# Kernel optimization log

Hardware: AMD Instinct MI355X
Metric: run time of the kernel (lower is better)

## Reference

```python
import jax, jax.numpy as jnp
import numpy as np

B, N = 4, 2048
VD, CD = 256, 64
H = 4
INNER = VD  # inner_ratio = 1
D = INNER // H  # head_dim = 64
EPS = 1e-5
RMS_EPS = 1e-6


def layer_norm(x, g, b):
    m = jnp.mean(x, axis=-1, keepdims=True)
    v = jnp.mean((x - m) ** 2, axis=-1, keepdims=True)
    return (x - m) * jax.lax.rsqrt(v + EPS) * g + b


def rms_norm(x, s):
    ms = jnp.mean(x * x, axis=-1, keepdims=True)
    return x * jax.lax.rsqrt(ms + RMS_EPS) * s


def split_heads(x):  # (b, n, h*d) -> (b, h, n, d)
    b, n, _ = x.shape
    return x.reshape(b, n, H, D).transpose(0, 2, 1, 3)


def setup_inputs() -> dict:
    key = jax.random.key(0)
    ks = jax.random.split(key, 10)
    w = lambda k, shp: jax.random.normal(k, shp, dtype=jnp.float32) * 0.02
    return {
        "V": jax.random.normal(ks[0], (B, N, VD), dtype=jnp.float32),
        "C": jax.random.normal(ks[1], (B, N, CD), dtype=jnp.float32),
        "vn_g": jnp.ones((VD,), jnp.float32), "vn_b": jnp.zeros((VD,), jnp.float32),
        "cn_g": jnp.ones((CD,), jnp.float32), "cn_b": jnp.zeros((CD,), jnp.float32),
        "W_vqk": w(ks[2], (VD, 2 * INNER)), "b_vqk": jnp.zeros((2 * INNER,), jnp.float32),
        "rms_v": jnp.ones((2 * INNER,), jnp.float32),
        "W_cqk": w(ks[3], (CD, 2 * INNER)), "b_cqk": jnp.zeros((2 * INNER,), jnp.float32),
        "rms_c": jnp.ones((2 * INNER,), jnp.float32),
        "W_vv": w(ks[4], (VD, INNER)), "b_vv": jnp.zeros((INNER,), jnp.float32),
        "W_cv": w(ks[5], (CD, INNER)), "b_cv": jnp.zeros((INNER,), jnp.float32),
        "W_ov": w(ks[6], (INNER, VD)), "b_ov": jnp.zeros((VD,), jnp.float32),
        "W_oc": w(ks[7], (INNER, CD)), "b_oc": jnp.zeros((CD,), jnp.float32),
    }


def reference(V, C, vn_g, vn_b, cn_g, cn_b, W_vqk, b_vqk, rms_v, W_cqk, b_cqk, rms_c,
              W_vv, b_vv, W_cv, b_cv, W_ov, b_ov, W_oc, b_oc):
    Vn = layer_norm(V, vn_g, vn_b)
    Cn = layer_norm(C, cn_g, cn_b)
    qkv = rms_norm(Vn @ W_vqk + b_vqk, rms_v)
    qkc = rms_norm(Cn @ W_cqk + b_cqk, rms_c)
    qv, kv = jnp.split(qkv, 2, axis=-1)
    qc, kc = jnp.split(qkc, 2, axis=-1)
    vv = Vn @ W_vv + b_vv
    vc = Cn @ W_cv + b_cv
    qv, kv, vv, qc, kc, vc = map(split_heads, (qv, kv, vv, qc, kc, vc))
    # shared attention map: softmax((QvKv^T + QcKc^T)/sqrt(d))
    scores = (jnp.einsum("bhnd,bhmd->bhnm", qv, kv)
              + jnp.einsum("bhnd,bhmd->bhnm", qc, kc)) / np.sqrt(D).astype(np.float32)
    attn = jax.nn.softmax(scores, axis=-1)
    out_v = jnp.einsum("bhnm,bhmd->bhnd", attn, vv).transpose(0, 2, 1, 3).reshape(B, N, INNER)
    out_c = jnp.einsum("bhnm,bhmd->bhnd", attn, vc).transpose(0, 2, 1, 3).reshape(B, N, INNER)
    return out_v @ W_ov + b_ov, out_c @ W_oc + b_oc
```

## Files before the change

### kernel.cpp

```cpp
#include <hip/hip_runtime.h>

typedef unsigned short u16;
typedef unsigned int   u32;
typedef short s16x8 __attribute__((ext_vector_type(8)));
typedef float f32x4 __attribute__((ext_vector_type(4)));

#define WS_STATSV 0
#define WS_STATSC 65536
#define WS_WT_VQK 131072
#define WS_WT_CQK 393216
#define WS_WT_VV  458752
#define WS_WT_CV  589824
#define WS_WT_OV  622592
#define WS_WT_OC  753664
#define WS_Q      786432
#define WS_K      9175040
#define WS_VT     17563648
#define WS_OV     25952256
#define WS_OC     30146560

__device__ __forceinline__ float bf2f(u16 h){
  union { u32 u; float f; } x; x.u = ((u32)h) << 16; return x.f;
}
__device__ __forceinline__ u16 f2bf(float f){
  union { float f; u32 u; } x; x.f = f;
  u32 u = x.u; u += 0x7fffu + ((u >> 16) & 1u);
  return (u16)(u >> 16);
}
__device__ __forceinline__ f32x4 mfma16(s16x8 a, s16x8 b, f32x4 c){
  return __builtin_amdgcn_mfma_f32_16x16x32_bf16(a, b, c, 0, 0, 0);
}
__device__ __forceinline__ void async16(const u16* g, u16* l){
  __builtin_amdgcn_global_load_lds(
      (const __attribute__((address_space(1))) u32*)(const void*)g,
      (__attribute__((address_space(3))) u32*)(void*)l, 16, 0, 0);
}

__global__ __launch_bounds__(256) void k_prep(const float* V, const float* C,
    const float* Wvqk, const float* Wcqk, const float* Wvv, const float* Wcv,
    const float* Wov, const float* Woc, char* ws){
  int bid = blockIdx.x;
  if (bid < 4096){
    int wid = threadIdx.x >> 6, lane = threadIdx.x & 63;
    float2* sV = (float2*)(ws + WS_STATSV);
    float2* sC = (float2*)(ws + WS_STATSC);
    float s = 0.f, s2 = 0.f; int row; float2* dst; float invn;
    if (bid < 2048){
      row = bid*4 + wid;
      const float4* p = (const float4*)(V + row*256);
      float4 v = p[lane];
      s = v.x+v.y+v.z+v.w; s2 = v.x*v.x+v.y*v.y+v.z*v.z+v.w*v.w;
      dst = sV; invn = 1.0f/256.0f;
    } else {
      row = (bid-2048)*4 + wid;
      float x = C[row*64 + lane];
      s = x; s2 = x*x;
      dst = sC; invn = 1.0f/64.0f;
    }
    for (int d=1; d<64; d<<=1){ s += __shfl_xor(s,d); s2 += __shfl_xor(s2,d); }
    if (lane == 0){
      float m = s*invn; float var = s2*invn - m*m; if (var < 0.f) var = 0.f;
      float rstd = rsqrtf(var + 1e-5f);
      float2 o; o.x = rstd; o.y = -m*rstd;
      dst[row] = o;
    }
  } else {
    int tb = bid - 4096;
    const float* src; u16* dst; int K, N, rel;
    if      (tb <  64){ src=Wvqk; dst=(u16*)(ws+WS_WT_VQK); K=256; N=512; rel=tb;     }
    else if (tb <  80){ src=Wcqk; dst=(u16*)(ws+WS_WT_CQK); K=64;  N=512; rel=tb-64;  }
    else if (tb < 112){ src=Wvv;  dst=(u16*)(ws+WS_WT_VV);  K=256; N=256; rel=tb-80;  }
    else if (tb < 120){ src=Wcv;  dst=(u16*)(ws+WS_WT_CV);  K=64;  N=256; rel=tb-112; }
    else if (tb < 152){ src=Wov;  dst=(u16*)(ws+WS_WT_OV);  K=256; N=256; rel=tb-120; }
    else              { src=Woc;  dst=(u16*)(ws+WS_WT_OC);  K=256; N=64;  rel=tb-152; }
    int e = rel*2048 + threadIdx.x*8;
    int k = e / N, n0 = e % N;
    float4 t0 = *(const float4*)(src + e);
    float4 t1 = *(const float4*)(src + e + 4);
    dst[(n0+0)*K + k] = f2bf(t0.x);
    dst[(n0+1)*K + k] = f2bf(t0.y);
    dst[(n0+2)*K + k] = f2bf(t0.z);
    dst[(n0+3)*K + k] = f2bf(t0.w);
    dst[(n0+4)*K + k] = f2bf(t1.x);
    dst[(n0+5)*K + k] = f2bf(t1.y);
    dst[(n0+6)*K + k] = f2bf(t1.z);
    dst[(n0+7)*K + k] = f2bf(t1.w);
  }
}

__device__ __forceinline__ s16x8 ln_frag(const float* A, const float* g, const float* bb,
                                         int base, int k0, float2 stt){
  float4 x0 = *(const float4*)(A + base + k0);
  float4 x1 = *(const float4*)(A + base + k0 + 4);
  float4 g0 = *(const float4*)(g + k0);
  float4 g1 = *(const float4*)(g + k0 + 4);
  float4 b0 = *(const float4*)(bb + k0);
  float4 b1 = *(const float4*)(bb + k0 + 4);
  s16x8 af;
  af[0] = (short)f2bf(fmaf(fmaf(x0.x, stt.x, stt.y), g0.x, b0.x));
  af[1] = (short)f2bf(fmaf(fmaf(x0.y, stt.x, stt.y), g0.y, b0.y));
  af[2] = (short)f2bf(fmaf(fmaf(x0.z, stt.x, stt.y), g0.z, b0.z));
  af[3] = (short)f2bf(fmaf(fmaf(x0.w, stt.x, stt.y), g0.w, b0.w));
  af[4] = (short)f2bf(fmaf(fmaf(x1.x, stt.x, stt.y), g1.x, b1.x));
  af[5] = (short)f2bf(fmaf(fmaf(x1.y, stt.x, stt.y), g1.y, b1.y));
  af[6] = (short)f2bf(fmaf(fmaf(x1.z, stt.x, stt.y), g1.z, b1.z));
  af[7] = (short)f2bf(fmaf(fmaf(x1.w, stt.x, stt.y), g1.w, b1.w));
  return af;
}

__global__ __launch_bounds__(256) void k_proj(const float* V, const float* C,
    const float* vg, const float* vb, const float* cgam, const float* cbet,
    const float* bvqk, const float* bcqk, const float* rmsv, const float* rmsc,
    const float* bvv, const float* bcv, char* ws){
  __shared__ float ssl[4][16];
  int bid = blockIdx.x;
  int tid = threadIdx.x, lane = tid & 63, w = tid >> 6;
  int c = lane & 15, q = lane >> 4;

  if (bid < 1024){
    bool csd = bid >= 512;
    int rb = (bid & 511) * 16;
    const float* A   = csd ? C : V;
    int K            = csd ? 64 : 256;
    const float2* st = (const float2*)(ws + (csd ? WS_STATSC : WS_STATSV));
    const float* g   = csd ? cgam : vg;
    const float* bb  = csd ? cbet : vb;
    const u16* Wt    = (const u16*)(ws + (csd ? WS_WT_CQK : WS_WT_VQK));
    const float* bias= csd ? bcqk : bvqk;
    const float* rms = csd ? rmsc : rmsv;
    int dOff         = csd ? 64 : 0;

    int row = rb + c;
    float2 stt = st[row];
    int j0 = w * 128;

    f32x4 acc[8];
    #pragma unroll
    for (int f=0; f<8; f++){ f32x4 z = {0.f,0.f,0.f,0.f}; acc[f] = z; }

    int nkc = K >> 5;
    for (int kc=0; kc<nkc; kc++){
      int k0 = kc*32 + q*8;
      s16x8 af = ln_frag(A, g, bb, row*K, k0, stt);
      #pragma unroll
      for (int f=0; f<8; f++){
        s16x8 bfr = *(const s16x8*)(Wt + (j0 + f*16 + c)*K + k0);
        acc[f] = mfma16(af, bfr, acc[f]);
      }
    }

    float ss[4] = {0.f,0.f,0.f,0.f};
    float rsv[8];
    #pragma unroll
    for (int f=0; f<8; f++){
      int j = j0 + f*16 + c;
      float bsv = bias[j]; rsv[f] = rms[j];
      #pragma unroll
      for (int i=0;i<4;i++){ acc[f][i] += bsv; ss[i] += acc[f][i]*acc[f][i]; }
    }
    #pragma unroll
    for (int d=1; d<16; d<<=1){
      #pragma unroll
      for (int i=0;i<4;i++) ss[i] += __shfl_xor(ss[i], d);
    }
    if (c == 0){
      #pragma unroll
      for (int i=0;i<4;i++) ssl[w][q*4 + i] = ss[i];
    }
    __syncthreads();
    float rmsr[4];
    #pragma unroll
    for (int i=0;i<4;i++){
      int rl = q*4 + i;
      float tot = ssl[0][rl] + ssl[1][rl] + ssl[2][rl] + ssl[3][rl];
      rmsr[i] = rsqrtf(tot * (1.0f/512.0f) + 1e-6f);
    }
    u16* dstb = (u16*)(ws + (w < 2 ? WS_Q : WS_K));
    float qs = (w < 2) ? 0.125f*1.44269504f : 1.0f;
    #pragma unroll
    for (int f=0; f<8; f++){
      int jj = (j0 + f*16 + c) & 255;
      int head = jj >> 6, dd = (jj & 63) + dOff;
      #pragma unroll
      for (int i=0;i<4;i++){
        int r = rb + q*4 + i;
        int b_ = r >> 11, n = r & 2047;
        dstb[((b_*4 + head)*2048 + n)*128 + dd] = f2bf(acc[f][i]*rmsr[i]*rsv[f]*qs);
      }
    }
  } else {
    int vb2 = bid - 1024;
    bool csd = vb2 >= 256;
    int rb = (vb2 & 255) * 32;
    const float* A   = csd ? C : V;
    int K            = csd ? 64 : 256;
    const float2* st = (const float2*)(ws + (csd ? WS_STATSC : WS_STATSV));
    const float* g   = csd ? cgam : vg;
    const float* bb  = csd ? cbet : vb;
    const u16* Wt    = (const u16*)(ws + (csd ? WS_WT_CV : WS_WT_VV));
    const float* bias= csd ? bcv : bvv;
    int dOff         = csd ? 64 : 0;

    int s = w & 1, cgp = w >> 1;
    int r0 = rb + s*16, row = r0 + c;
    float2 stt = st[row];
    int j0 = cgp * 128;

    f32x4 acc[8];
    #pragma unroll
    for (int f=0; f<8; f++){ f32x4 z = {0.f,0.f,0.f,0.f}; acc[f] = z; }

    int nkc = K >> 5;
    for (int kc=0; kc<nkc; kc++){
      int k0 = kc*32 + q*8;
      s16x8 af = ln_frag(A, g, bb, row*K, k0, stt);
      #pragma unroll
      for (int f=0; f<8; f++){
        s16x8 bfr = *(const s16x8*)(Wt + (j0 + f*16 + c)*K + k0);
        acc[f] = mfma16(af, bfr, acc[f]);
      }
    }
    u16* vt = (u16*)(ws + WS_VT);
    int r = r0 + q*4;
    int b_ = r >> 11, n = r & 2047;
    int m = n & 31;
    int nper = (n & ~31) | (((m & 15) >> 2)*8 + (m >> 4)*4);
    #pragma unroll
    for (int f=0; f<8; f++){
      int j = j0 + f*16 + c;
      float bv_ = bias[j];
      int head = j >> 6, dd = (j & 63) + dOff;
      ushort4 pk;
      pk.x = f2bf(acc[f][0] + bv_); pk.y = f2bf(acc[f][1] + bv_);
      pk.z = f2bf(acc[f][2] + bv_); pk.w = f2bf(acc[f][3] + bv_);
      *(ushort4*)(vt + ((b_*4 + head)*128 + dd)*2048 + nper) = pk;
    }
  }
}

__global__ __launch_bounds__(256, 2) void k_attn(char* ws){
  const u16* Qw = (const u16*)(ws + WS_Q);
  const u16* Kw = (const u16*)(ws + WS_K);
  const u16* Vt = (const u16*)(ws + WS_VT);
  u16* Ov = (u16*)(ws + WS_OV);
  u16* Oc = (u16*)(ws + WS_OC);
  __shared__ char smem[65536];
  u16* sm16 = (u16*)smem;

  int bh = blockIdx.x & 15, qb = blockIdx.x >> 4;
  int tid = threadIdx.x, lane = tid & 63, w = tid >> 6;
  int c = lane & 15, q = lane >> 4;
  int g = w & 1, h = w >> 1, ht = tid & 127;
  int qr0 = qb*64 + g*32;

  s16x8 qf[2][4];
  #pragma unroll
  for (int s=0;s<2;s++)
    #pragma unroll
    for (int kc=0;kc<4;kc++)
      qf[s][kc] = *(const s16x8*)(Qw + (bh*2048 + qr0 + s*16 + c)*128 + kc*32 + q*8);

  const u16* ksrc[4]; const u16* vsrc[4];
  #pragma unroll
  for (int i=0;i<4;i++){
    int sc = i*128 + ht;
    { int r = sc >> 4, j = (sc & 15) ^ (r & 15);
      ksrc[i] = Kw + (bh*2048 + r)*128 + j*8; }
    { int r = sc >> 2, j = (sc & 3) ^ ((r >> 1) & 3);
      vsrc[i] = Vt + (bh*128 + r)*2048 + j*8; }
  }

  f32x4 o[2][8];
  float lsum[2] = {0.f, 0.f};
  #pragma unroll
  for (int s=0;s<2;s++)
    #pragma unroll
    for (int f8=0;f8<8;f8++){ f32x4 z = {0.f,0.f,0.f,0.f}; o[s][f8] = z; }

  auto stage = [&](int buf, int t){
    u16* kd = sm16 + (h*2+buf)*4096;
    u16* vd = sm16 + 16384 + (h*2+buf)*4096;
    #pragma unroll
    for (int i=0;i<4;i++){
      async16(ksrc[i] + t*4096, kd + (i*128+ht)*8);
      async16(vsrc[i] + t*32,   vd + (i*128+ht)*8);
    }
  };

  auto step = [&](int bi, int tt){
    int t = h*32 + tt;
    __syncthreads();
    if (tt < 31) stage(bi^1, t+1);

    const u16* kb = sm16 + (h*2+bi)*4096;
    const u16* vb = sm16 + 16384 + (h*2+bi)*4096;
    s16x8 kf[2][4];
    #pragma unroll
    for (int f=0;f<2;f++)
      #pragma unroll
      for (int kc=0;kc<4;kc++)
        kf[f][kc] = *(const s16x8*)(kb + ((f*16+c)*16 + (((kc*4+q) ^ c) & 15))*8);
    s16x8 vf[8];
    #pragma unroll
    for (int f8=0;f8<8;f8++)
      vf[f8] = *(const s16x8*)(vb + ((f8*16+c)*4 + ((q ^ ((c>>1)&3)) & 3))*8);

    f32x4 sfr[2][2];
    #pragma unroll
    for (int s=0;s<2;s++)
      #pragma unroll
      for (int f=0;f<2;f++){ f32x4 z = {0.f,0.f,0.f,0.f}; sfr[s][f] = z; }
    #pragma unroll
    for (int s=0;s<2;s++)
      #pragma unroll
      for (int f=0;f<2;f++)
        #pragma unroll
        for (int kc=0;kc<4;kc++)
          sfr[s][f] = mfma16(kf[f][kc], qf[s][kc], sfr[s][f]);

    #pragma unroll
    for (int s=0;s<2;s++){
      float p0 = exp2f(sfr[s][0][0]), p1 = exp2f(sfr[s][0][1]);
      float p2 = exp2f(sfr[s][0][2]), p3 = exp2f(sfr[s][0][3]);
      float p4 = exp2f(sfr[s][1][0]), p5 = exp2f(sfr[s][1][1]);
      float p6 = exp2f(sfr[s][1][2]), p7 = exp2f(sfr[s][1][3]);
      lsum[s] += ((p0+p1)+(p2+p3)) + ((p4+p5)+(p6+p7));
      union { u32 u[4]; s16x8 v; } pa;
      pa.u[0] = (u32)f2bf(p0) | ((u32)f2bf(p1) << 16);
      pa.u[1] = (u32)f2bf(p2) | ((u32)f2bf(p3) << 16);
      pa.u[2] = (u32)f2bf(p4) | ((u32)f2bf(p5) << 16);
      pa.u[3] = (u32)f2bf(p6) | ((u32)f2bf(p7) << 16);
      #pragma unroll
      for (int f8=0;f8<8;f8++)
        o[s][f8] = mfma16(pa.v, vf[f8], o[s][f8]);
    }
  };

  stage(0, h*32);
  for (int tt=0; tt<32; tt+=2){
    step(0, tt);
    step(1, tt+1);
  }

  __syncthreads();
  float* mg = (float*)smem;
  if (h == 1){
    float* d = mg + (g*64 + lane)*67;
    #pragma unroll
    for (int s=0;s<2;s++)
      #pragma unroll
      for (int f8=0;f8<8;f8++)
        #pragma unroll
        for (int i=0;i<4;i++) d[(s*8+f8)*4 + i] = o[s][f8][i];
    d[64] = lsum[0]; d[65] = lsum[1];
  }
  __syncthreads();
  if (h == 0){
    float* d = mg + (g*64 + lane)*67;
    #pragma unroll
    for (int s=0;s<2;s++)
      #pragma unroll
      for (int f8=0;f8<8;f8++)
        #pragma unroll
        for (int i=0;i<4;i++) o[s][f8][i] += d[(s*8+f8)*4 + i];
    lsum[0] += d[64]; lsum[1] += d[65];

    #pragma unroll
    for (int s=0;s<2;s++){
      lsum[s] += __shfl_xor(lsum[s], 16);
      lsum[s] += __shfl_xor(lsum[s], 32);
    }

    int b_ = bh >> 2, hh = bh & 3;
    #pragma unroll
    for (int s=0;s<2;s++){
      float inv[4];
      #pragma unroll
      for (int i=0;i<4;i++) inv[i] = 1.0f/__shfl(lsum[s], q*4 + i);
      #pragma unroll
      for (int f8=0;f8<8;f8++){
        int col = f8*16 + c;
        u16* dst = (col < 64) ? Ov : Oc;
        int ddim = col & 63;
        #pragma unroll
        for (int i=0;i<4;i++){
          int n = qr0 + s*16 + q*4 + i;
          dst[(b_*2048 + n)*256 + hh*64 + ddim] = f2bf(o[s][f8][i]*inv[i]);
        }
      }
    }
  }
}

__global__ __launch_bounds__(256) void k_out(const u16* Av, const u16* Wtv, const float* bv,
                                             const u16* Ac, const u16* Wtc, const float* bc,
                                             float* out){
  int bid = blockIdx.x;
  int tid = threadIdx.x, lane = tid & 63, w = tid >> 6;
  int c = lane & 15, q = lane >> 4;
  if (bid < 512){
    int rb = bid * 16;
    int row = rb + c;
    int j0 = w * 64;
    f32x4 acc[4];
    #pragma unroll
    for (int f=0; f<4; f++){ f32x4 z = {0.f,0.f,0.f,0.f}; acc[f] = z; }
    for (int kc=0; kc<8; kc++){
      int k0 = kc*32 + q*8;
      s16x8 af = *(const s16x8*)(Av + row*256 + k0);
      #pragma unroll
      for (int f=0; f<4; f++){
        s16x8 bfr = *(const s16x8*)(Wtv + (j0 + f*16 + c)*256 + k0);
        acc[f] = mfma16(af, bfr, acc[f]);
      }
    }
    #pragma unroll
    for (int f=0; f<4; f++){
      int j = j0 + f*16 + c;
      float bb = bv[j];
      #pragma unroll
      for (int i=0;i<4;i++)
        out[(rb + q*4 + i)*256 + j] = acc[f][i] + bb;
    }
  } else {
    int rb = (bid - 512) * 64;
    int r0 = rb + w*16, row = r0 + c;
    f32x4 acc[4];
    #pragma unroll
    for (int f=0; f<4; f++){ f32x4 z = {0.f,0.f,0.f,0.f}; acc[f] = z; }
    for (int kc=0; kc<8; kc++){
      int k0 = kc*32 + q*8;
      s16x8 af = *(const s16x8*)(Ac + row*256 + k0);
      #pragma unroll
      for (int f=0; f<4; f++){
        s16x8 bfr = *(const s16x8*)(Wtc + (f*16 + c)*256 + k0);
        acc[f] = mfma16(af, bfr, acc[f]);
      }
    }
    float* oc = out + 2097152;
    #pragma unroll
    for (int f=0; f<4; f++){
      int j = f*16 + c;
      float bb = bc[j];
      #pragma unroll
      for (int i=0;i<4;i++)
        oc[(r0 + q*4 + i)*64 + j] = acc[f][i] + bb;
    }
  }
}

extern "C" void kernel_launch(void* const* d_in, const int* in_sizes, int n_in,
                              void* d_out, int out_size, void* d_ws, size_t ws_size,
                              hipStream_t stream){
  (void)in_sizes; (void)n_in; (void)out_size; (void)ws_size;
  const float* V    = (const float*)d_in[0];
  const float* C    = (const float*)d_in[1];
  const float* vng  = (const float*)d_in[2];
  const float* vnb  = (const float*)d_in[3];
  const float* cng  = (const float*)d_in[4];
  const float* cnb  = (const float*)d_in[5];
  const float* Wvqk = (const float*)d_in[6];
  const float* bvqk = (const float*)d_in[7];
  const float* rmsv = (const float*)d_in[8];
  const float* Wcqk = (const float*)d_in[9];
  const float* bcqk = (const float*)d_in[10];
  const float* rmsc = (const float*)d_in[11];
  const float* Wvv  = (const float*)d_in[12];
  const float* bvv  = (const float*)d_in[13];
  const float* Wcv  = (const float*)d_in[14];
  const float* bcv  = (const float*)d_in[15];
  const float* Wov  = (const float*)d_in[16];
  const float* bov  = (const float*)d_in[17];
  const float* Woc  = (const float*)d_in[18];
  const float* boc  = (const float*)d_in[19];
  char* ws = (char*)d_ws;
  float* out = (float*)d_out;

  k_prep<<<4256, 256, 0, stream>>>(V, C, Wvqk, Wcqk, Wvv, Wcv, Wov, Woc, ws);
  k_proj<<<1536, 256, 0, stream>>>(V, C, vng, vnb, cng, cnb,
                                   bvqk, bcqk, rmsv, rmsc, bvv, bcv, ws);
  k_attn<<<512, 256, 0, stream>>>(ws);
  k_out<<<640, 256, 0, stream>>>((const u16*)(ws + WS_OV), (const u16*)(ws + WS_WT_OV), bov,
                                 (const u16*)(ws + WS_OC), (const u16*)(ws + WS_WT_OC), boc,
                                 out);
}
```

Before: 215.1 us.

## Pre-pack K/V in MFMA fragment order and load directly from global

The layer norm is now applied once in the prep kernel, which writes normalized bf16 V and C rows into the workspace; the projection kernel reads these instead of recomputing the norm for every column block. The projection kernel now stores K and V directly in the per-lane MFMA fragment order that attention consumes. The attention kernel then drops its LDS staging and barriers and double-buffers tiles in registers with coalesced 16-byte global loads. The trade is higher register pressure in attention and the loss of LDS sharing between waves, so each wave fetches its own K/V tiles from L2. The normalized activations reuse the WS_OV/WS_OC buffers, which attention later overwrites.

```diff
diff --git a/kernel.cpp b/kernel.cpp
--- a/kernel.cpp
+++ b/kernel.cpp
@@ -30,39 +30,39 @@
 __device__ __forceinline__ f32x4 mfma16(s16x8 a, s16x8 b, f32x4 c){
   return __builtin_amdgcn_mfma_f32_16x16x32_bf16(a, b, c, 0, 0, 0);
 }
-__device__ __forceinline__ void async16(const u16* g, u16* l){
-  __builtin_amdgcn_global_load_lds(
-      (const __attribute__((address_space(1))) u32*)(const void*)g,
-      (__attribute__((address_space(3))) u32*)(void*)l, 16, 0, 0);
-}
 
 __global__ __launch_bounds__(256) void k_prep(const float* V, const float* C,
+    const float* vng, const float* vnb, const float* cng, const float* cnb,
     const float* Wvqk, const float* Wcqk, const float* Wvv, const float* Wcv,
     const float* Wov, const float* Woc, char* ws){
   int bid = blockIdx.x;
   if (bid < 4096){
     int wid = threadIdx.x >> 6, lane = threadIdx.x & 63;
-    float2* sV = (float2*)(ws + WS_STATSV);
-    float2* sC = (float2*)(ws + WS_STATSC);
-    float s = 0.f, s2 = 0.f; int row; float2* dst; float invn;
     if (bid < 2048){
-      row = bid*4 + wid;
+      int row = bid*4 + wid;
       const float4* p = (const float4*)(V + row*256);
       float4 v = p[lane];
-      s = v.x+v.y+v.z+v.w; s2 = v.x*v.x+v.y*v.y+v.z*v.z+v.w*v.w;
-      dst = sV; invn = 1.0f/256.0f;
+      float s = v.x+v.y+v.z+v.w, s2 = v.x*v.x+v.y*v.y+v.z*v.z+v.w*v.w;
+      for (int d=1; d<64; d<<=1){ s += __shfl_xor(s,d); s2 += __shfl_xor(s2,d); }
+      float m = s*(1.0f/256.0f); float var = s2*(1.0f/256.0f) - m*m; if (var < 0.f) var = 0.f;
+      float rstd = rsqrtf(var + 1e-5f), nb = -m*rstd;
+      float4 gg = ((const float4*)vng)[lane];
+      float4 bb = ((const float4*)vnb)[lane];
+      ushort4 pk;
+      pk.x = f2bf(fmaf(fmaf(v.x, rstd, nb), gg.x, bb.x));
+      pk.y = f2bf(fmaf(fmaf(v.y, rstd, nb), gg.y, bb.y));
+      pk.z = f2bf(fmaf(fmaf(v.z, rstd, nb), gg.z, bb.z));
+      pk.w = f2bf(fmaf(fmaf(v.w, rstd, nb), gg.w, bb.w));
+      *(ushort4*)((u16*)(ws + WS_OV) + row*256 + lane*4) = pk;
     } else {
-      row = (bid-2048)*4 + wid;
+      int row = (bid-2048)*4 + wid;
       float x = C[row*64 + lane];
-      s = x; s2 = x*x;
-      dst = sC; invn = 1.0f/64.0f;
-    }
-    for (int d=1; d<64; d<<=1){ s += __shfl_xor(s,d); s2 += __shfl_xor(s2,d); }
-    if (lane == 0){
-      float m = s*invn; float var = s2*invn - m*m; if (var < 0.f) var = 0.f;
+      float s = x, s2 = x*x;
+      for (int d=1; d<64; d<<=1){ s += __shfl_xor(s,d); s2 += __shfl_xor(s2,d); }
+      float m = s*(1.0f/64.0f); float var = s2*(1.0f/64.0f) - m*m; if (var < 0.f) var = 0.f;
       float rstd = rsqrtf(var + 1e-5f);
-      float2 o; o.x = rstd; o.y = -m*rstd;
-      dst[row] = o;
+      float xn = fmaf(fmaf(x, rstd, -m*rstd), cng[lane], cnb[lane]);
+      ((u16*)(ws + WS_OC))[row*64 + lane] = f2bf(xn);
     }
   } else {
     int tb = bid - 4096;
@@ -88,30 +88,8 @@
   }
 }
 
-__device__ __forceinline__ s16x8 ln_frag(const float* A, const float* g, const float* bb,
-                                         int base, int k0, float2 stt){
-  float4 x0 = *(const float4*)(A + base + k0);
-  float4 x1 = *(const float4*)(A + base + k0 + 4);
-  float4 g0 = *(const float4*)(g + k0);
-  float4 g1 = *(const float4*)(g + k0 + 4);
-  float4 b0 = *(const float4*)(bb + k0);
-  float4 b1 = *(const float4*)(bb + k0 + 4);
-  s16x8 af;
-  af[0] = (short)f2bf(fmaf(fmaf(x0.x, stt.x, stt.y), g0.x, b0.x));
-  af[1] = (short)f2bf(fmaf(fmaf(x0.y, stt.x, stt.y), g0.y, b0.y));
-  af[2] = (short)f2bf(fmaf(fmaf(x0.z, stt.x, stt.y), g0.z, b0.z));
-  af[3] = (short)f2bf(fmaf(fmaf(x0.w, stt.x, stt.y), g0.w, b0.w));
-  af[4] = (short)f2bf(fmaf(fmaf(x1.x, stt.x, stt.y), g1.x, b1.x));
-  af[5] = (short)f2bf(fmaf(fmaf(x1.y, stt.x, stt.y), g1.y, b1.y));
-  af[6] = (short)f2bf(fmaf(fmaf(x1.z, stt.x, stt.y), g1.z, b1.z));
-  af[7] = (short)f2bf(fmaf(fmaf(x1.w, stt.x, stt.y), g1.w, b1.w));
-  return af;
-}
-
-__global__ __launch_bounds__(256) void k_proj(const float* V, const float* C,
-    const float* vg, const float* vb, const float* cgam, const float* cbet,
-    const float* bvqk, const float* bcqk, const float* rmsv, const float* rmsc,
-    const float* bvv, const float* bcv, char* ws){
+__global__ __launch_bounds__(256) void k_proj(const float* bvqk, const float* bcqk,
+    const float* rmsv, const float* rmsc, const float* bvv, const float* bcv, char* ws){
   __shared__ float ssl[4][16];
   int bid = blockIdx.x;
   int tid = threadIdx.x, lane = tid & 63, w = tid >> 6;
@@ -120,18 +98,14 @@
   if (bid < 1024){
     bool csd = bid >= 512;
     int rb = (bid & 511) * 16;
-    const float* A   = csd ? C : V;
+    const u16* An    = (const u16*)(ws + (csd ? WS_OC : WS_OV));
     int K            = csd ? 64 : 256;
-    const float2* st = (const float2*)(ws + (csd ? WS_STATSC : WS_STATSV));
-    const float* g   = csd ? cgam : vg;
-    const float* bb  = csd ? cbet : vb;
     const u16* Wt    = (const u16*)(ws + (csd ? WS_WT_CQK : WS_WT_VQK));
     const float* bias= csd ? bcqk : bvqk;
     const float* rms = csd ? rmsc : rmsv;
     int dOff         = csd ? 64 : 0;
 
     int row = rb + c;
-    float2 stt = st[row];
     int j0 = w * 128;
 
     f32x4 acc[8];
@@ -141,7 +115,7 @@
     int nkc = K >> 5;
     for (int kc=0; kc<nkc; kc++){
       int k0 = kc*32 + q*8;
-      s16x8 af = ln_frag(A, g, bb, row*K, k0, stt);
+      s16x8 af = *(const s16x8*)(An + row*K + k0);
       #pragma unroll
       for (int f=0; f<8; f++){
         s16x8 bfr = *(const s16x8*)(Wt + (j0 + f*16 + c)*K + k0);
@@ -175,35 +149,49 @@
       float tot = ssl[0][rl] + ssl[1][rl] + ssl[2][rl] + ssl[3][rl];
       rmsr[i] = rsqrtf(tot * (1.0f/512.0f) + 1e-6f);
     }
-    u16* dstb = (u16*)(ws + (w < 2 ? WS_Q : WS_K));
-    float qs = (w < 2) ? 0.125f*1.44269504f : 1.0f;
-    #pragma unroll
-    for (int f=0; f<8; f++){
-      int jj = (j0 + f*16 + c) & 255;
-      int head = jj >> 6, dd = (jj & 63) + dOff;
-      #pragma unroll
-      for (int i=0;i<4;i++){
-        int r = rb + q*4 + i;
-        int b_ = r >> 11, n = r & 2047;
-        dstb[((b_*4 + head)*2048 + n)*128 + dd] = f2bf(acc[f][i]*rmsr[i]*rsv[f]*qs);
+    if (w < 2){
+      u16* dstb = (u16*)(ws + WS_Q);
+      const float qs = 0.125f*1.44269504f;
+      #pragma unroll
+      for (int f=0; f<8; f++){
+        int jj = (j0 + f*16 + c) & 255;
+        int head = jj >> 6, dd = (jj & 63) + dOff;
+        #pragma unroll
+        for (int i=0;i<4;i++){
+          int r = rb + q*4 + i;
+          int b_ = r >> 11, n = r & 2047;
+          dstb[((b_*4 + head)*2048 + n)*128 + dd] = f2bf(acc[f][i]*rmsr[i]*rsv[f]*qs);
+        }
+      }
+    } else {
+      u16* kfb = (u16*)(ws + WS_K);
+      #pragma unroll
+      for (int f=0; f<8; f++){
+        int jj = (j0 + f*16 + c) & 255;
+        int head = jj >> 6, dd = (jj & 63) + dOff;
+        int kcK = dd >> 5, qK = (dd >> 3) & 3, eK = dd & 7;
+        #pragma unroll
+        for (int i=0;i<4;i++){
+          int r = rb + q*4 + i;
+          int b_ = r >> 11, n = r & 2047;
+          int t = n >> 5, fK = (n >> 4) & 1, cK = n & 15;
+          kfb[(b_*4 + head)*262144 + t*4096 + (fK*4 + kcK)*512 + (qK*16 + cK)*8 + eK]
+            = f2bf(acc[f][i]*rmsr[i]*rsv[f]);
+        }
       }
     }
   } else {
     int vb2 = bid - 1024;
     bool csd = vb2 >= 256;
     int rb = (vb2 & 255) * 32;
-    const float* A   = csd ? C : V;
+    const u16* An    = (const u16*)(ws + (csd ? WS_OC : WS_OV));
     int K            = csd ? 64 : 256;
-    const float2* st = (const float2*)(ws + (csd ? WS_STATSC : WS_STATSV));
-    const float* g   = csd ? cgam : vg;
-    const float* bb  = csd ? cbet : vb;
     const u16* Wt    = (const u16*)(ws + (csd ? WS_WT_CV : WS_WT_VV));
     const float* bias= csd ? bcv : bvv;
     int dOff         = csd ? 64 : 0;
 
     int s = w & 1, cgp = w >> 1;
     int r0 = rb + s*16, row = r0 + c;
-    float2 stt = st[row];
     int j0 = cgp * 128;
 
     f32x4 acc[8];
@@ -213,44 +201,45 @@
     int nkc = K >> 5;
     for (int kc=0; kc<nkc; kc++){
       int k0 = kc*32 + q*8;
-      s16x8 af = ln_frag(A, g, bb, row*K, k0, stt);
+      s16x8 af = *(const s16x8*)(An + row*K + k0);
       #pragma unroll
       for (int f=0; f<8; f++){
         s16x8 bfr = *(const s16x8*)(Wt + (j0 + f*16 + c)*K + k0);
         acc[f] = mfma16(af, bfr, acc[f]);
       }
     }
-    u16* vt = (u16*)(ws + WS_VT);
+    u16* vfb = (u16*)(ws + WS_VT);
     int r = r0 + q*4;
     int b_ = r >> 11, n = r & 2047;
-    int m = n & 31;
-    int nper = (n & ~31) | (((m & 15) >> 2)*8 + (m >> 4)*4);
+    int t = n >> 5, m = n & 31;
+    int qV = (m < 16) ? (m >> 2) : ((m >> 2) - 4);
+    int e0 = (m < 16) ? 0 : 4;
     #pragma unroll
     for (int f=0; f<8; f++){
       int j = j0 + f*16 + c;
       float bv_ = bias[j];
       int head = j >> 6, dd = (j & 63) + dOff;
+      int f8 = dd >> 4, cV = dd & 15;
       ushort4 pk;
       pk.x = f2bf(acc[f][0] + bv_); pk.y = f2bf(acc[f][1] + bv_);
       pk.z = f2bf(acc[f][2] + bv_); pk.w = f2bf(acc[f][3] + bv_);
-      *(ushort4*)(vt + ((b_*4 + head)*128 + dd)*2048 + nper) = pk;
+      *(ushort4*)(vfb + (b_*4 + head)*262144 + t*4096 + f8*512 + (qV*16 + cV)*8 + e0) = pk;
     }
   }
 }
 
 __global__ __launch_bounds__(256, 2) void k_attn(char* ws){
   const u16* Qw = (const u16*)(ws + WS_Q);
-  const u16* Kw = (const u16*)(ws + WS_K);
-  const u16* Vt = (const u16*)(ws + WS_VT);
+  const u16* KF = (const u16*)(ws + WS_K);
+  const u16* VF = (const u16*)(ws + WS_VT);
   u16* Ov = (u16*)(ws + WS_OV);
   u16* Oc = (u16*)(ws + WS_OC);
-  __shared__ char smem[65536];
-  u16* sm16 = (u16*)smem;
+  __shared__ float mg[2][64][67];
 
   int bh = blockIdx.x & 15, qb = blockIdx.x >> 4;
   int tid = threadIdx.x, lane = tid & 63, w = tid >> 6;
   int c = lane & 15, q = lane >> 4;
-  int g = w & 1, h = w >> 1, ht = tid & 127;
+  int g = w & 1, h = w >> 1;
   int qr0 = qb*64 + g*32;
 
   s16x8 qf[2][4];
@@ -260,15 +249,8 @@
     for (int kc=0;kc<4;kc++)
       qf[s][kc] = *(const s16x8*)(Qw + (bh*2048 + qr0 + s*16 + c)*128 + kc*32 + q*8);
 
-  const u16* ksrc[4]; const u16* vsrc[4];
-  #pragma unroll
-  for (int i=0;i<4;i++){
-    int sc = i*128 + ht;
-    { int r = sc >> 4, j = (sc & 15) ^ (r & 15);
-      ksrc[i] = Kw + (bh*2048 + r)*128 + j*8; }
-    { int r = sc >> 2, j = (sc & 3) ^ ((r >> 1) & 3);
-      vsrc[i] = Vt + (bh*128 + r)*2048 + j*8; }
-  }
+  const u16* kb = KF + bh*262144 + h*131072 + lane*8;
+  const u16* vb = VF + bh*262144 + h*131072 + lane*8;
 
   f32x4 o[2][8];
   float lsum[2] = {0.f, 0.f};
@@ -277,34 +259,22 @@
     #pragma unroll
     for (int f8=0;f8<8;f8++){ f32x4 z = {0.f,0.f,0.f,0.f}; o[s][f8] = z; }
 
-  auto stage = [&](int buf, int t){
-    u16* kd = sm16 + (h*2+buf)*4096;
-    u16* vd = sm16 + 16384 + (h*2+buf)*4096;
-    #pragma unroll
-    for (int i=0;i<4;i++){
-      async16(ksrc[i] + t*4096, kd + (i*128+ht)*8);
-      async16(vsrc[i] + t*32,   vd + (i*128+ht)*8);
-    }
+  s16x8 kA[2][4], vA[8], kB[2][4], vB[8];
+
+  auto loadT = [&](s16x8 (&kf)[2][4], s16x8 (&vf)[8], int tt){
+    const u16* kt = kb + tt*4096;
+    const u16* vt = vb + tt*4096;
+    #pragma unroll
+    for (int f=0;f<2;f++)
+      #pragma unroll
+      for (int kc=0;kc<4;kc++)
+        kf[f][kc] = *(const s16x8*)(kt + (f*4+kc)*512);
+    #pragma unroll
+    for (int f8=0;f8<8;f8++)
+      vf[f8] = *(const s16x8*)(vt + f8*512);
   };
 
-  auto step = [&](int bi, int tt){
-    int t = h*32 + tt;
-    __syncthreads();
-    if (tt < 31) stage(bi^1, t+1);
-
-    const u16* kb = sm16 + (h*2+bi)*4096;
-    const u16* vb = sm16 + 16384 + (h*2+bi)*4096;
-    s16x8 kf[2][4];
-    #pragma unroll
-    for (int f=0;f<2;f++)
-      #pragma unroll
-      for (int kc=0;kc<4;kc++)
-        kf[f][kc] = *(const s16x8*)(kb + ((f*16+c)*16 + (((kc*4+q) ^ c) & 15))*8);
-    s16x8 vf[8];
-    #pragma unroll
-    for (int f8=0;f8<8;f8++)
-      vf[f8] = *(const s16x8*)(vb + ((f8*16+c)*4 + ((q ^ ((c>>1)&3)) & 3))*8);
-
+  auto comp = [&](const s16x8 (&kf)[2][4], const s16x8 (&vf)[8]){
     f32x4 sfr[2][2];
     #pragma unroll
     for (int s=0;s<2;s++)
@@ -336,16 +306,17 @@
     }
   };
 
-  stage(0, h*32);
+  loadT(kA, vA, 0);
   for (int tt=0; tt<32; tt+=2){
-    step(0, tt);
-    step(1, tt+1);
+    loadT(kB, vB, tt+1);
+    comp(kA, vA);
+    if (tt+2 < 32) loadT(kA, vA, tt+2);
+    comp(kB, vB);
   }
 
   __syncthreads();
-  float* mg = (float*)smem;
   if (h == 1){
-    float* d = mg + (g*64 + lane)*67;
+    float* d = &mg[g][lane][0];
     #pragma unroll
     for (int s=0;s<2;s++)
       #pragma unroll
@@ -356,7 +327,7 @@
   }
   __syncthreads();
   if (h == 0){
-    float* d = mg + (g*64 + lane)*67;
+    float* d = &mg[g][lane][0];
     #pragma unroll
     for (int s=0;s<2;s++)
       #pragma unroll
@@ -476,9 +447,9 @@
   char* ws = (char*)d_ws;
   float* out = (float*)d_out;
 
-  k_prep<<<4256, 256, 0, stream>>>(V, C, Wvqk, Wcqk, Wvv, Wcv, Wov, Woc, ws);
-  k_proj<<<1536, 256, 0, stream>>>(V, C, vng, vnb, cng, cnb,
-                                   bvqk, bcqk, rmsv, rmsc, bvv, bcv, ws);
+  k_prep<<<4256, 256, 0, stream>>>(V, C, vng, vnb, cng, cnb,
+                                   Wvqk, Wcqk, Wvv, Wcv, Wov, Woc, ws);
+  k_proj<<<1536, 256, 0, stream>>>(bvqk, bcqk, rmsv, rmsc, bvv, bcv, ws);
   k_attn<<<512, 256, 0, stream>>>(ws);
   k_out<<<640, 256, 0, stream>>>((const u16*)(ws + WS_OV), (const u16*)(ws + WS_WT_OV), bov,
                                  (const u16*)(ws + WS_OC), (const u16*)(ws + WS_WT_OC), boc,
```

Result: faster. 203.3 us (-5.5%).
